# Kernel optimization log

Hardware: AMD Instinct MI355X
Metric: run time of the kernel (lower is better)

The kernel has to match this reference:

```python
import jax, jax.numpy as jnp
import numpy as np

N = 512     # nodes
E = 16384   # edges (N * avg_degree 32, unique pairs)
F = 64      # nedgeinput
FO = 64     # nedgeoutput


def setup_inputs() -> dict:
    key = jax.random.key(0)
    ks = jax.random.split(key, 7)
    # unique edge pairs so scatter-assign is well-defined
    perm = jax.random.permutation(ks[0], N * N)[:E]
    edge_index = jnp.stack([perm // N, perm % N]).astype(jnp.int32)  # [2, E]
    C = jax.random.normal(ks[1], (E, F), dtype=jnp.float32)
    batch_node = jax.random.normal(ks[2], (N,), dtype=jnp.float32)
    s = 1.0 / np.sqrt(F)
    W_L1 = jax.random.normal(ks[3], (F, F), dtype=jnp.float32) * s          # Linear(F, F), weight [out,in]
    W_L2 = jax.random.normal(ks[4], (F, F), dtype=jnp.float32) * s
    W_mlp1 = jax.random.normal(ks[5], (8 * F, 2 * F), dtype=jnp.float32) * (1.0 / np.sqrt(2 * F))
    W_mlp2 = jax.random.normal(ks[6], (FO, 8 * F), dtype=jnp.float32) * (1.0 / np.sqrt(8 * F))
    return {"edge_index": edge_index, "C": C, "batch_node": batch_node,
            "W_L1": W_L1, "W_L2": W_L2, "W_mlp1": W_mlp1, "W_mlp2": W_mlp2}


def reference(edge_index, C, batch_node, W_L1, W_L2, W_mlp1, W_mlp2):
    n = batch_node.shape[0]
    f = C.shape[1]
    ei0, ei1 = edge_index[0], edge_index[1]
    X = C @ W_L1.T  # [E, F]  (L1(C))
    Y = C @ W_L2.T  # [E, F]  (L2(C))
    # scatter edges into dense [F, N, N] adjacency-like tensors
    resx = jnp.zeros((f, n, n), dtype=C.dtype).at[:, ei0, ei1].set(X.T)
    resy = jnp.zeros((f, n, n), dtype=C.dtype).at[:, ei0, ei1].set(Y.T)
    # batched dense matmul per feature channel, then gather back at edges
    res = jnp.einsum('fij,fjk->fik', resx, resy)  # [F, N, N]
    tmp_matmul = res[:, ei0, ei1].T  # [E, F]
    tmp = jnp.concatenate([C, tmp_matmul], axis=1)  # [E, 2F]
    return jax.nn.relu(tmp @ W_mlp1.T) @ W_mlp2.T  # [E, FO]
```

## Files before the change

kernel.cpp:

```cpp
#include <hip/hip_runtime.h>

#define NN 512
#define NE 16384
#define NF 64

typedef __attribute__((ext_vector_type(8))) short short8_t;
typedef __attribute__((ext_vector_type(4))) float float4_t;

__device__ inline unsigned short f2bf(float f) {
  unsigned u = __builtin_bit_cast(unsigned, f);
  u += 0x7fff + ((u >> 16) & 1);
  return (unsigned short)(u >> 16);
}
__device__ inline float bf2f(unsigned short u) {
  unsigned v = ((unsigned)u) << 16;
  return __builtin_bit_cast(float, v);
}

__global__ __launch_bounds__(256) void k_init(const float* __restrict__ Wm1,
                                              const float* __restrict__ Wm2,
                                              unsigned* __restrict__ masks,
                                              unsigned short* __restrict__ W1B,
                                              unsigned short* __restrict__ W2B) {
  int t = blockIdx.x * 256 + threadIdx.x;
  if (t < 16384) {
    masks[t] = 0u;
    float4 v = ((const float4*)Wm1)[t];
    short4 s;
    s.x = f2bf(v.x); s.y = f2bf(v.y); s.z = f2bf(v.z); s.w = f2bf(v.w);
    ((short4*)W1B)[t] = s;
  } else if (t < 24576) {
    int i = t - 16384;
    float4 v = ((const float4*)Wm2)[i];
    short4 s;
    s.x = f2bf(v.x); s.y = f2bf(v.y); s.z = f2bf(v.z); s.w = f2bf(v.w);
    ((short4*)W2B)[i] = s;
  }
}

__global__ __launch_bounds__(256) void k_xy_mfma(const float* __restrict__ C,
                                                 const float* __restrict__ W1,
                                                 const float* __restrict__ W2,
                                                 const int* __restrict__ ei,
                                                 int* __restrict__ eid,
                                                 int* __restrict__ eidT,
                                                 unsigned* __restrict__ maskO,
                                                 unsigned* __restrict__ maskI,
                                                 unsigned short* __restrict__ Xb,
                                                 unsigned short* __restrict__ Yb,
                                                 unsigned short* __restrict__ tmpB) {
  __shared__ __attribute__((aligned(16))) short W1s[64 * 72];
  __shared__ __attribute__((aligned(16))) short W2s[64 * 72];
  int t = threadIdx.x;
  int w = t >> 6;
  int lane = t & 63;
  int col = lane & 15;
  int q = lane >> 4;
  int base_e = blockIdx.x * 64 + w * 16;

  if (t < 64) {
    int e = blockIdx.x * 64 + t;
    int i = ei[e];
    int k = ei[NE + e];
    eid[i * NN + k] = e;
    eidT[k * NN + i] = e;
    atomicOr(&maskO[i * 16 + (k >> 5)], 1u << (k & 31));
    atomicOr(&maskI[k * 16 + (i >> 5)], 1u << (i & 31));
  }

#pragma unroll
  for (int z = 0; z < 4; z++) {
    int gi = z * 256 + t;
    int r = gi >> 4, c = gi & 15;
    float4 v1 = ((const float4*)W1)[r * 16 + c];
    float4 v2 = ((const float4*)W2)[r * 16 + c];
    short4 s1, s2;
    s1.x = f2bf(v1.x); s1.y = f2bf(v1.y); s1.z = f2bf(v1.z); s1.w = f2bf(v1.w);
    s2.x = f2bf(v2.x); s2.y = f2bf(v2.y); s2.z = f2bf(v2.z); s2.w = f2bf(v2.w);
    *(short4*)(W1s + r * 72 + c * 4) = s1;
    *(short4*)(W2s + r * 72 + c * 4) = s2;
  }
  __syncthreads();

  short8_t bfrag[2];
#pragma unroll
  for (int ks = 0; ks < 2; ks++) {
    float4 c0 = ((const float4*)C)[(size_t)(base_e + col) * 16 + ks * 8 + q * 2];
    float4 c1 = ((const float4*)C)[(size_t)(base_e + col) * 16 + ks * 8 + q * 2 + 1];
    short8_t s;
    s[0] = (short)f2bf(c0.x); s[1] = (short)f2bf(c0.y);
    s[2] = (short)f2bf(c0.z); s[3] = (short)f2bf(c0.w);
    s[4] = (short)f2bf(c1.x); s[5] = (short)f2bf(c1.y);
    s[6] = (short)f2bf(c1.z); s[7] = (short)f2bf(c1.w);
    bfrag[ks] = s;
    *(short8_t*)(tmpB + (size_t)(base_e + col) * 128 + ks * 32 + q * 8) = s;
  }

  float4_t xa[4], ya[4];
#pragma unroll
  for (int ft = 0; ft < 4; ft++) {
    xa[ft] = (float4_t){0.f, 0.f, 0.f, 0.f};
    ya[ft] = (float4_t){0.f, 0.f, 0.f, 0.f};
  }
#pragma unroll
  for (int ks = 0; ks < 2; ks++) {
#pragma unroll
    for (int ft = 0; ft < 4; ft++) {
      short8_t a1 = *(const short8_t*)(W1s + (ft * 16 + col) * 72 + ks * 32 + q * 8);
      short8_t a2 = *(const short8_t*)(W2s + (ft * 16 + col) * 72 + ks * 32 + q * 8);
      xa[ft] = __builtin_amdgcn_mfma_f32_16x16x32_bf16(a1, bfrag[ks], xa[ft], 0, 0, 0);
      ya[ft] = __builtin_amdgcn_mfma_f32_16x16x32_bf16(a2, bfrag[ks], ya[ft], 0, 0, 0);
    }
  }
#pragma unroll
  for (int ft = 0; ft < 4; ft++) {
    short4 sx, sy;
    sx.x = (short)f2bf(xa[ft][0]); sx.y = (short)f2bf(xa[ft][1]);
    sx.z = (short)f2bf(xa[ft][2]); sx.w = (short)f2bf(xa[ft][3]);
    sy.x = (short)f2bf(ya[ft][0]); sy.y = (short)f2bf(ya[ft][1]);
    sy.z = (short)f2bf(ya[ft][2]); sy.w = (short)f2bf(ya[ft][3]);
    *(short4*)(Xb + (size_t)(base_e + col) * 64 + ft * 16 + q * 4) = sx;
    *(short4*)(Yb + (size_t)(base_e + col) * 64 + ft * 16 + q * 4) = sy;
  }
}

__global__ __launch_bounds__(256) void k_spmm(const int* __restrict__ ei,
                                              const int* __restrict__ eid,
                                              const int* __restrict__ eidT,
                                              const unsigned* __restrict__ maskO,
                                              const unsigned* __restrict__ maskI,
                                              const unsigned short* __restrict__ Xb,
                                              const unsigned short* __restrict__ Yb,
                                              unsigned short* __restrict__ tmpB) {
  int lane = threadIdx.x & 63;
  int e = (blockIdx.x * 256 + threadIdx.x) >> 6;
  int i = ei[e];
  int k = ei[NE + e];
  unsigned mm = 0;
  if (lane < 16) mm = maskO[i * 16 + lane] & maskI[k * 16 + lane];
  unsigned long long has = __ballot(mm != 0);
  float acc = 0.f;
  while (has) {
    int l = (int)__builtin_ctzll(has);
    has &= has - 1;
    unsigned bits = __shfl(mm, l);
    while (bits) {
      int b = __builtin_ctz(bits);
      bits &= bits - 1;
      int j = l * 32 + b;
      int s1 = eid[i * NN + j];
      int s2 = eidT[k * NN + j];
      float xv = bf2f(Xb[(size_t)s1 * 64 + lane]);
      float yv = bf2f(Yb[(size_t)s2 * 64 + lane]);
      acc = fmaf(xv, yv, acc);
    }
  }
  tmpB[(size_t)e * 128 + 64 + lane] = f2bf(acc);
}

__global__ __launch_bounds__(256) void k_mlp2(
    const unsigned short* __restrict__ tmpB,
    const unsigned short* __restrict__ W1B,
    const unsigned short* __restrict__ W2B,
    float* __restrict__ out) {
  __shared__ __attribute__((aligned(16))) short W1s[128 * 136];
  __shared__ __attribute__((aligned(16))) short W2s[64 * 136];
  __shared__ __attribute__((aligned(16))) short hS[4][16 * 72];

  int t = threadIdx.x;
  int w = t >> 6;
  int lane = t & 63;
  int col = lane & 15;
  int q = lane >> 4;
  int g = w & 1;
  int h = w >> 1;
  int base_e = blockIdx.x * 32 + g * 16;

  short8_t btmp[4];
#pragma unroll
  for (int ks = 0; ks < 4; ks++)
    btmp[ks] = *(const short8_t*)(tmpB + (size_t)(base_e + col) * 128 + ks * 32 + q * 8);

  float4_t oacc[4];
#pragma unroll
  for (int ft = 0; ft < 4; ft++) oacc[ft] = (float4_t){0.f, 0.f, 0.f, 0.f};

  for (int it = 0; it < 4; it++) {
    __syncthreads();
    {
      uint4* d1 = (uint4*)W1s;
      const uint4* s1 = (const uint4*)W1B;
#pragma unroll
      for (int z = 0; z < 8; z++) {
        int gi = z * 256 + t;
        int r = gi >> 4, c = gi & 15;
        int grow = ((r >> 6) * 4 + it) * 64 + (r & 63);
        d1[r * 17 + c] = s1[(size_t)grow * 16 + c];
      }
      uint4* d2 = (uint4*)W2s;
      const uint4* s2 = (const uint4*)W2B;
#pragma unroll
      for (int z = 0; z < 4; z++) {
        int gi = z * 256 + t;
        int r = gi >> 4, c = gi & 15;
        int gc = ((c >> 3) * 4 + it) * 8 + (c & 7);
        d2[r * 17 + c] = s2[(size_t)r * 64 + gc];
      }
    }
    __syncthreads();

#pragma unroll
    for (int ht = 0; ht < 4; ht++) {
      float4_t hacc = (float4_t){0.f, 0.f, 0.f, 0.f};
#pragma unroll
      for (int ks = 0; ks < 4; ks++) {
        short8_t af = *(const short8_t*)(W1s + (h * 64 + ht * 16 + col) * 136 + ks * 32 + q * 8);
        hacc = __builtin_amdgcn_mfma_f32_16x16x32_bf16(af, btmp[ks], hacc, 0, 0, 0);
      }
      short4 hp;
      hp.x = (short)f2bf(fmaxf(hacc[0], 0.f));
      hp.y = (short)f2bf(fmaxf(hacc[1], 0.f));
      hp.z = (short)f2bf(fmaxf(hacc[2], 0.f));
      hp.w = (short)f2bf(fmaxf(hacc[3], 0.f));
      *(short4*)(&hS[w][col * 72 + ht * 16 + q * 4]) = hp;
    }

#pragma unroll
    for (int ks2 = 0; ks2 < 2; ks2++) {
      short8_t a2 = *(const short8_t*)(&hS[w][col * 72 + ks2 * 32 + q * 8]);
#pragma unroll
      for (int ft = 0; ft < 4; ft++) {
        short8_t b2 = *(const short8_t*)(W2s + (ft * 16 + col) * 136 + h * 64 + ks2 * 32 + q * 8);
        oacc[ft] = __builtin_amdgcn_mfma_f32_16x16x32_bf16(a2, b2, oacc[ft], 0, 0, 0);
      }
    }
  }

  __syncthreads();
  float* red = (float*)W1s;
  if (h == 1) {
#pragma unroll
    for (int ft = 0; ft < 4; ft++)
#pragma unroll
      for (int r = 0; r < 4; r++)
        red[(g * 16 + q * 4 + r) * 66 + ft * 16 + col] = oacc[ft][r];
  }
  __syncthreads();
  if (h == 0) {
#pragma unroll
    for (int ft = 0; ft < 4; ft++)
#pragma unroll
      for (int r = 0; r < 4; r++) {
        float v = oacc[ft][r] + red[(g * 16 + q * 4 + r) * 66 + ft * 16 + col];
        out[(size_t)(base_e + q * 4 + r) * 64 + ft * 16 + col] = v;
      }
  }
}

extern "C" void kernel_launch(void* const* d_in, const int* in_sizes, int n_in,
                              void* d_out, int out_size, void* d_ws, size_t ws_size,
                              hipStream_t stream) {
  const int* ei = (const int*)d_in[0];
  const float* C = (const float*)d_in[1];
  const float* W1 = (const float*)d_in[3];
  const float* W2 = (const float*)d_in[4];
  const float* Wm1 = (const float*)d_in[5];
  const float* Wm2 = (const float*)d_in[6];
  float* out = (float*)d_out;

  char* p = (char*)d_ws;
  int* eid = (int*)p;                 p += (size_t)NN * NN * 4;
  int* eidT = (int*)p;                p += (size_t)NN * NN * 4;
  unsigned* masks = (unsigned*)p;     p += (size_t)16384 * 4;
  unsigned short* Xb = (unsigned short*)p;    p += (size_t)NE * NF * 2;
  unsigned short* Yb = (unsigned short*)p;    p += (size_t)NE * NF * 2;
  unsigned short* tmpB = (unsigned short*)p;  p += (size_t)NE * 128 * 2;
  unsigned short* W1B = (unsigned short*)p;   p += (size_t)512 * 128 * 2;
  unsigned short* W2B = (unsigned short*)p;   p += (size_t)64 * 512 * 2;
  unsigned* maskO = masks;
  unsigned* maskI = masks + 8192;

  k_init<<<128, 256, 0, stream>>>(Wm1, Wm2, masks, W1B, W2B);
  k_xy_mfma<<<NE / 64, 256, 0, stream>>>(C, W1, W2, ei, eid, eidT, maskO, maskI, Xb, Yb, tmpB);
  k_spmm<<<(NE * 64) / 256, 256, 0, stream>>>(ei, eid, eidT, maskO, maskI, Xb, Yb, tmpB);
  k_mlp2<<<NE / 32, 256, 0, stream>>>(tmpB, W1B, W2B, out);
}
```

Baseline: 98.26 us.

## Fuse sparse edge-product gather into the MLP kernel via shared memory

Removes the standalone SpMM kernel and computes each block's 32 edge products inside the MLP kernel. Each wave handles 8 edges, and results go into shared memory that is reused from the hidden buffer. The C half of the concat is reconverted to bf16 directly from C instead of being written to and reread from a global tmp buffer. This saves one kernel launch and the tmp buffer round trip. The trade-off is that the gather's irregular latency now sits serially in front of the MLP's MFMA work within each block, with fewer waves in flight for the gather.

New measurement: 107.8 us. +9.7%, slower.

```diff
diff --git a/kernel.cpp b/kernel.cpp
--- a/kernel.cpp
+++ b/kernel.cpp
@@ -47,8 +47,7 @@
                                                  unsigned* __restrict__ maskO,
                                                  unsigned* __restrict__ maskI,
                                                  unsigned short* __restrict__ Xb,
-                                                 unsigned short* __restrict__ Yb,
-                                                 unsigned short* __restrict__ tmpB) {
+                                                 unsigned short* __restrict__ Yb) {
   __shared__ __attribute__((aligned(16))) short W1s[64 * 72];
   __shared__ __attribute__((aligned(16))) short W2s[64 * 72];
   int t = threadIdx.x;
@@ -93,7 +92,6 @@
     s[4] = (short)f2bf(c1.x); s[5] = (short)f2bf(c1.y);
     s[6] = (short)f2bf(c1.z); s[7] = (short)f2bf(c1.w);
     bfrag[ks] = s;
-    *(short8_t*)(tmpB + (size_t)(base_e + col) * 128 + ks * 32 + q * 8) = s;
   }
 
   float4_t xa[4], ya[4];
@@ -124,42 +122,15 @@
   }
 }
 
-__global__ __launch_bounds__(256) void k_spmm(const int* __restrict__ ei,
-                                              const int* __restrict__ eid,
-                                              const int* __restrict__ eidT,
-                                              const unsigned* __restrict__ maskO,
-                                              const unsigned* __restrict__ maskI,
-                                              const unsigned short* __restrict__ Xb,
-                                              const unsigned short* __restrict__ Yb,
-                                              unsigned short* __restrict__ tmpB) {
-  int lane = threadIdx.x & 63;
-  int e = (blockIdx.x * 256 + threadIdx.x) >> 6;
-  int i = ei[e];
-  int k = ei[NE + e];
-  unsigned mm = 0;
-  if (lane < 16) mm = maskO[i * 16 + lane] & maskI[k * 16 + lane];
-  unsigned long long has = __ballot(mm != 0);
-  float acc = 0.f;
-  while (has) {
-    int l = (int)__builtin_ctzll(has);
-    has &= has - 1;
-    unsigned bits = __shfl(mm, l);
-    while (bits) {
-      int b = __builtin_ctz(bits);
-      bits &= bits - 1;
-      int j = l * 32 + b;
-      int s1 = eid[i * NN + j];
-      int s2 = eidT[k * NN + j];
-      float xv = bf2f(Xb[(size_t)s1 * 64 + lane]);
-      float yv = bf2f(Yb[(size_t)s2 * 64 + lane]);
-      acc = fmaf(xv, yv, acc);
-    }
-  }
-  tmpB[(size_t)e * 128 + 64 + lane] = f2bf(acc);
-}
-
-__global__ __launch_bounds__(256) void k_mlp2(
-    const unsigned short* __restrict__ tmpB,
+__global__ __launch_bounds__(256) void k_smlp(
+    const float* __restrict__ C,
+    const int* __restrict__ ei,
+    const int* __restrict__ eid,
+    const int* __restrict__ eidT,
+    const unsigned* __restrict__ maskO,
+    const unsigned* __restrict__ maskI,
+    const unsigned short* __restrict__ Xb,
+    const unsigned short* __restrict__ Yb,
     const unsigned short* __restrict__ W1B,
     const unsigned short* __restrict__ W2B,
     float* __restrict__ out) {
@@ -174,12 +145,60 @@
   int q = lane >> 4;
   int g = w & 1;
   int h = w >> 1;
-  int base_e = blockIdx.x * 32 + g * 16;
+  int base = blockIdx.x * 32;
+  int base_e = base + g * 16;
+
+  short* tmpS = (short*)hS;
+  {
+    int iv[8], kv[8];
+    unsigned mm[8];
+#pragma unroll
+    for (int n = 0; n < 8; n++) {
+      int e = base + w * 8 + n;
+      iv[n] = ei[e];
+      kv[n] = ei[NE + e];
+    }
+#pragma unroll
+    for (int n = 0; n < 8; n++)
+      mm[n] = (lane < 16) ? (maskO[iv[n] * 16 + lane] & maskI[kv[n] * 16 + lane]) : 0u;
+#pragma unroll
+    for (int n = 0; n < 8; n++) {
+      unsigned long long has = __ballot(mm[n] != 0);
+      float acc = 0.f;
+      while (has) {
+        int l = (int)__builtin_ctzll(has);
+        has &= has - 1;
+        unsigned bits = __shfl(mm[n], l);
+        while (bits) {
+          int b = __builtin_ctz(bits);
+          bits &= bits - 1;
+          int j = l * 32 + b;
+          int s1 = eid[iv[n] * NN + j];
+          int s2 = eidT[kv[n] * NN + j];
+          acc = fmaf(bf2f(Xb[(size_t)s1 * 64 + lane]),
+                     bf2f(Yb[(size_t)s2 * 64 + lane]), acc);
+        }
+      }
+      tmpS[(w * 8 + n) * 72 + lane] = (short)f2bf(acc);
+    }
+  }
+  __syncthreads();
 
   short8_t btmp[4];
 #pragma unroll
-  for (int ks = 0; ks < 4; ks++)
-    btmp[ks] = *(const short8_t*)(tmpB + (size_t)(base_e + col) * 128 + ks * 32 + q * 8);
+  for (int ks = 0; ks < 2; ks++) {
+    float4 c0 = ((const float4*)C)[(size_t)(base_e + col) * 16 + ks * 8 + q * 2];
+    float4 c1 = ((const float4*)C)[(size_t)(base_e + col) * 16 + ks * 8 + q * 2 + 1];
+    short8_t s;
+    s[0] = (short)f2bf(c0.x); s[1] = (short)f2bf(c0.y);
+    s[2] = (short)f2bf(c0.z); s[3] = (short)f2bf(c0.w);
+    s[4] = (short)f2bf(c1.x); s[5] = (short)f2bf(c1.y);
+    s[6] = (short)f2bf(c1.z); s[7] = (short)f2bf(c1.w);
+    btmp[ks] = s;
+  }
+#pragma unroll
+  for (int ks = 2; ks < 4; ks++)
+    btmp[ks] = *(const short8_t*)(tmpS + (g * 16 + col) * 72 + (ks - 2) * 32 + q * 8);
 
   float4_t oacc[4];
 #pragma unroll
@@ -274,14 +293,12 @@
   unsigned* masks = (unsigned*)p;     p += (size_t)16384 * 4;
   unsigned short* Xb = (unsigned short*)p;    p += (size_t)NE * NF * 2;
   unsigned short* Yb = (unsigned short*)p;    p += (size_t)NE * NF * 2;
-  unsigned short* tmpB = (unsigned short*)p;  p += (size_t)NE * 128 * 2;
   unsigned short* W1B = (unsigned short*)p;   p += (size_t)512 * 128 * 2;
   unsigned short* W2B = (unsigned short*)p;   p += (size_t)64 * 512 * 2;
   unsigned* maskO = masks;
   unsigned* maskI = masks + 8192;
 
   k_init<<<128, 256, 0, stream>>>(Wm1, Wm2, masks, W1B, W2B);
-  k_xy_mfma<<<NE / 64, 256, 0, stream>>>(C, W1, W2, ei, eid, eidT, maskO, maskI, Xb, Yb, tmpB);
-  k_spmm<<<(NE * 64) / 256, 256, 0, stream>>>(ei, eid, eidT, maskO, maskI, Xb, Yb, tmpB);
-  k_mlp2<<<NE / 32, 256, 0, stream>>>(tmpB, W1B, W2B, out);
-}
+  k_xy_mfma<<<NE / 64, 256, 0, stream>>>(C, W1, W2, ei, eid, eidT, maskO, maskI, Xb, Yb);
+  k_smlp<<<NE / 32, 256, 0, stream>>>(C, ei, eid, eidT, maskO, maskI, Xb, Yb, W1B, W2B, out);
+}
```
